# Kernel tuning notes

Hardware: AMD Instinct MI355X
Metric: run time of the kernel (lower is better)

The kernel has to match this reference:

```python
import jax, jax.numpy as jnp
from jax import lax
import numpy as np

N_NODES = 8192
N_FEATURES = 1024
N_FILTRATIONS = 4
HIDDEN_DIM = 64
MAX_DEG = 8            # fixed out-degree used when generating edge_list
N_EDGES = N_NODES * MAX_DEG


def setup_inputs() -> dict:
    key = jax.random.key(0)
    ks = jax.random.split(key, 10)
    X = jax.random.normal(ks[0], (N_NODES, N_FEATURES), dtype=jnp.float32)
    # directed edge list, exactly MAX_DEG out-edges per node
    src = jnp.repeat(jnp.arange(N_NODES, dtype=jnp.int32), MAX_DEG)
    dst = jax.random.randint(ks[1], (N_EDGES,), 0, N_NODES, dtype=jnp.int32)
    edge_list = jnp.stack([src, dst], axis=0)
    # filtrations_nn: Linear(n_features,32) -> ReLU -> Linear(32,n_filtrations)
    W1 = jax.random.normal(ks[2], (32, N_FEATURES), dtype=jnp.float32) * 0.05
    b1 = jnp.zeros((32,), jnp.float32)
    W2 = jax.random.normal(ks[3], (N_FILTRATIONS, 32), dtype=jnp.float32) * 0.05
    b2 = jnp.zeros((N_FILTRATIONS,), jnp.float32)
    # deep sets: theta = Linear(2*n_filtrations, hidden), rho = Linear(1, n_features)
    Wt = jax.random.normal(ks[4], (HIDDEN_DIM, 2 * N_FILTRATIONS), dtype=jnp.float32) * 0.05
    bt = jnp.zeros((HIDDEN_DIM,), jnp.float32)
    Wr = jax.random.normal(ks[5], (N_FEATURES, 1), dtype=jnp.float32) * 0.05
    br = jnp.zeros((N_FEATURES,), jnp.float32)
    return {"X": X, "edge_list": edge_list, "W1": W1, "b1": b1, "W2": W2,
            "b2": b2, "Wt": Wt, "bt": bt, "Wr": Wr, "br": br}


def uf_find(parent, node):
    # chase parent pointers until a root (parent[v] == v)
    return lax.while_loop(lambda v: parent[v] != v, lambda v: parent[v], node)


def build_neighbor_table(edge_list, n_nodes, max_deg):
    # padded CSR-style neighbor table (n_nodes, max_deg), -1 = no edge
    src = edge_list[0].astype(jnp.int32)
    dst = edge_list[1].astype(jnp.int32)
    e = src.shape[0]
    order_e = jnp.argsort(src)  # stable
    src_s, dst_s = src[order_e], dst[order_e]
    counts = jnp.zeros(n_nodes, jnp.int32).at[src].add(1)
    offsets = jnp.concatenate([jnp.zeros(1, jnp.int32), jnp.cumsum(counts)[:-1].astype(jnp.int32)])
    slot = jnp.arange(e, dtype=jnp.int32) - offsets[src_s]
    return jnp.full((n_nodes, max_deg), -1, jnp.int32).at[src_s, slot].set(dst_s)


def persistence_dim0(values, nbr_table):
    """0-dim persistence via sequential union-find with elder rule.
    Row for sort-position j: (birth=j, death=step when the component born at j is absorbed).
    Returned indexed by node id (diagram[order[j]] = row j), matching the torch code."""
    n = values.shape[0]
    order = jnp.argsort(values).astype(jnp.int32)  # filtration order
    pos = jnp.zeros(n, jnp.int32).at[order].set(jnp.arange(n, dtype=jnp.int32))  # rank
    parent0 = jnp.arange(n, dtype=jnp.int32)
    deaths0 = jnp.zeros(n, jnp.float32)

    def step_fn(carry, sv):
        parent, deaths = carry
        s, vertex = sv
        nbrs = nbr_table[vertex]

        def edge_body(k, pc):
            parent, deaths = pc
            u = nbrs[k]
            u_c = jnp.maximum(u, 0)
            valid = (u >= 0) & (pos[u_c] <= s)  # neighbor already activated
            u_eff = jnp.where(valid, u_c, vertex)
            r1 = uf_find(parent, vertex)
            r2 = uf_find(parent, u_eff)
            parent = parent.at[vertex].set(r1).at[u_eff].set(r2)  # path compression
            merge = r1 != r2
            older_is_r1 = pos[r1] < pos[r2]
            absorbed = jnp.where(older_is_r1, r2, r1)   # younger root dies (elder rule)
            survivor = jnp.where(older_is_r1, r1, r2)
            parent = parent.at[absorbed].set(jnp.where(merge, survivor, absorbed))
            dp = pos[absorbed]
            deaths = deaths.at[dp].set(jnp.where(merge, s.astype(jnp.float32), deaths[dp]))
            return (parent, deaths)

        parent, deaths = lax.fori_loop(0, MAX_DEG, edge_body, (parent, deaths))
        return (parent, deaths), None

    (_, deaths), _ = lax.scan(step_fn, (parent0, deaths0),
                              (jnp.arange(n, dtype=jnp.int32), order))
    # finalize: undying components -> inf in the original; use finite cap n for numerics
    deaths = jnp.where(deaths == 0.0, jnp.float32(n), deaths)
    births = jnp.arange(n, dtype=jnp.float32)
    diag_sorted = jnp.stack([births, deaths], axis=1)  # (n, 2), row j = sort position j
    return jnp.zeros((n, 2), jnp.float32).at[order].set(diag_sorted)


def reference(X, edge_list, W1, b1, W2, b2, Wt, bt, Wr, br):
    n = X.shape[0]
    # filtrations_nn
    h = jax.nn.relu(X @ W1.T + b1)
    filt = h @ W2.T + b2                      # (n, n_filtrations)
    filt_ng = lax.stop_gradient(filt)         # diagram is piecewise constant in filt
    nbr_table = build_neighbor_table(edge_list, n, MAX_DEG)
    pds = [persistence_dim0(filt_ng[:, i], nbr_table) for i in range(N_FILTRATIONS)]
    pd = jnp.stack(pds, axis=0).transpose(1, 0, 2).reshape(n, 2 * N_FILTRATIONS)
    # DeepSetsAggregation(theta, rho) with index=zeros(hidden_dim), dim=1:
    theta = pd @ Wt.T + bt                    # (n, hidden)
    pooled = jnp.sum(theta, axis=1, keepdims=True)  # segment-sum of dim 1 into one bucket
    x_hat = pooled @ Wr.T + br                # (n, n_features)
    return X + x_hat
```

## Files before the change

### kernel.cpp

```cpp
#include <hip/hip_runtime.h>

#define N_NODES     8192
#define N_FEAT      1024
#define N_FILT      4
#define MAXDEG      8
#define BLK         256
#define NB          (N_NODES / BLK)

__global__ __launch_bounds__(256) void filt_kernel(
    const float* __restrict__ X, const float* __restrict__ W1,
    const float* __restrict__ b1, const float* __restrict__ W2,
    const float* __restrict__ b2, float* __restrict__ filtT)
{
    const int node = blockIdx.x * 8 + (threadIdx.x >> 5);
    const int h    = threadIdx.x & 31;
    const float* xr = X  + (size_t)node * N_FEAT;
    const float* wr = W1 + (size_t)h    * N_FEAT;
    float acc = 0.f;
    for (int j = 0; j < N_FEAT; j += 4) {
        float4 xv = *reinterpret_cast<const float4*>(xr + j);
        float4 wv = *reinterpret_cast<const float4*>(wr + j);
        acc += xv.x * wv.x + xv.y * wv.y + xv.z * wv.z + xv.w * wv.w;
    }
    float hv = fmaxf(acc + b1[h], 0.f);
    #pragma unroll
    for (int fo = 0; fo < N_FILT; ++fo) {
        float v = hv * W2[fo * 32 + h];
        for (int off = 16; off; off >>= 1) v += __shfl_xor(v, off, 32);
        if (h == 0) filtT[fo * N_NODES + node] = v + b2[fo];
    }
}

__global__ void wsum_kernel(const float* __restrict__ Wt,
                            const float* __restrict__ bt,
                            float* __restrict__ wsum)
{
    int t = threadIdx.x;
    if (t < 8) {
        float s = 0.f;
        for (int hh = 0; hh < 64; ++hh) s += Wt[hh * 8 + t];
        wsum[t] = s;
    } else if (t == 8) {
        float s = 0.f;
        for (int hh = 0; hh < 64; ++hh) s += bt[hh];
        wsum[8] = s;
    }
}

__global__ __launch_bounds__(256) void rank_partial_kernel(
    const float* __restrict__ filtT, unsigned short* __restrict__ partial)
{
    const int b  = blockIdx.x;
    const int f  = b >> 7;
    const int cs = (b >> 5) & 3;
    const int cv = b & 31;
    const int v  = (cv << 8) + threadIdx.x;
    const float myv = filtT[(f << 13) + v];

    __shared__ float4 tile[512];
    const float4* src = reinterpret_cast<const float4*>(filtT + (f << 13) + cs * 2048);
    for (int i = threadIdx.x; i < 512; i += 256) tile[i] = src[i];
    __syncthreads();

    int cnt = 0;
    const int ubase = cs * 2048;
    #pragma unroll 4
    for (int j = 0; j < 512; ++j) {
        float4 wv = tile[j];
        int u = ubase + j * 4;
        cnt += (wv.x < myv) || (wv.x == myv && (u + 0) < v);
        cnt += (wv.y < myv) || (wv.y == myv && (u + 1) < v);
        cnt += (wv.z < myv) || (wv.z == myv && (u + 2) < v);
        cnt += (wv.w < myv) || (wv.w == myv && (u + 3) < v);
    }
    partial[((f * 4 + cs) << 13) + v] = (unsigned short)cnt;
}

__global__ __launch_bounds__(256) void rank_final_kernel(
    const unsigned short* __restrict__ partial,
    unsigned short* __restrict__ pos16, unsigned short* __restrict__ order16)
{
    int g = blockIdx.x * 256 + threadIdx.x;
    int f = g >> 13, v = g & 8191;
    int r = (int)partial[((f * 4 + 0) << 13) + v]
          + (int)partial[((f * 4 + 1) << 13) + v]
          + (int)partial[((f * 4 + 2) << 13) + v]
          + (int)partial[((f * 4 + 3) << 13) + v];
    pos16[(f << 13) + v] = (unsigned short)r;
    order16[(f << 13) + r] = (unsigned short)v;
}

__global__ __launch_bounds__(256) void etable_kernel(
    const unsigned short* __restrict__ order16,
    const unsigned short* __restrict__ pos16,
    const int* __restrict__ edge_dst,
    unsigned short* __restrict__ et)
{
    const int f  = blockIdx.x >> 5;
    const int e0 = ((blockIdx.x & 31) << 11);
    for (int i = threadIdx.x; i < 2048; i += 256) {
        int e = e0 + i;
        int s = e >> 3, k = e & 7;
        int v = (int)order16[(f << 13) + s];
        int u = edge_dst[v * MAXDEG + k];
        int q = (int)pos16[(f << 13) + u];
        et[(size_t)f * (N_NODES * MAXDEG) + e] = (unsigned short)(q < s ? q : s);
    }
}

__device__ __forceinline__ int row8min(int v) {
    int t = min(v, __builtin_amdgcn_mov_dpp(v, 0xB1, 0xF, 0xF, true));
    t = min(t, __builtin_amdgcn_mov_dpp(t, 0x4E, 0xF, 0xF, true));
    t = min(t, __builtin_amdgcn_mov_dpp(t, 0x141, 0xF, 0xF, true));
    return t;
}

__device__ __forceinline__ void chase8m(volatile unsigned int* vpd, int (&pk)[8]) {
    unsigned msk = 0;
    for (;;) {
        bool all = true;
        #pragma unroll
        for (int k = 0; k < 8; ++k) {
            if (!(msk & (1u << k))) {
                int q = (int)(vpd[pk[k]] & 0xffffu);
                if (q == pk[k]) msk |= (1u << k);
                else { pk[k] = q; all = false; }
            }
        }
        if (all) break;
    }
}

__global__ __launch_bounds__(256) void persist_kernel(
    const unsigned short* __restrict__ et,
    const unsigned short* __restrict__ pos16,
    unsigned short* __restrict__ death16)
{
    const int f    = blockIdx.x;
    const int tid  = threadIdx.x;
    const int lane = tid & 63;
    const int w    = tid >> 6;

    __shared__ unsigned int   s_pd[N_NODES];
    __shared__ unsigned short s_r16[2][BLK][8];
    __shared__ unsigned char  s_flag[2][BLK];
    __shared__ unsigned short s_list[2][BLK];
    __shared__ int s_wc[2][4];
    volatile unsigned int* vpd = s_pd;

    for (int v = tid; v < N_NODES; v += 256) s_pd[v] = (unsigned)v;
    __syncthreads();

    const unsigned short* etf = et + (size_t)f * (N_NODES * MAXDEG);

    for (int it = 0; it <= NB; ++it) {
        const int buf = it & 1;

        if (w == 0) {
            if (it > 0) {
                const int pbuf = (it - 1) & 1;
                const int plo  = (it - 1) * BLK;
                const int total = s_wc[pbuf][0] + s_wc[pbuf][1]
                                + s_wc[pbuf][2] + s_wc[pbuf][3];
                const int g    = lane >> 3;
                const int slot = lane & 7;
                for (int base = 0; base < total; base += 8) {
                    int idx = base + g;
                    if (idx >= total) idx = total - 1;
                    const int t = (int)s_list[pbuf][idx];
                    int p = (int)s_r16[pbuf][t][slot];
                    for (;;) {
                        int q = (int)(vpd[p] & 0xffffu);
                        if (__all(q == p)) break;
                        p = q;
                    }
                    const int gmax = (total - base < 8) ? (total - base) : 8;
                    bool kprev = false;
                    for (int gg = 0; gg < gmax; ++gg) {
                        if (kprev) {
                            for (;;) {
                                int q = (int)(vpd[p] & 0xffffu);
                                if (__all(q == p)) break;
                                p = q;
                            }
                        }
                        int m = row8min(p);
                        const bool ing  = (g == gg);
                        const bool kill = ing && (p != m);
                        kprev = (__ballot(kill) != 0ull);
                        if (kill)
                            vpd[p] = (unsigned)m | ((unsigned)(plo + t) << 16);
                    }
                }
            }
        } else if (it < NB) {
            const int lo = it * BLK;
            const int h  = tid - 64;
            #pragma unroll
            for (int rep = 0; rep < 2; ++rep) {
                const int sl = (rep == 0) ? h : (192 + h);
                if (rep == 1 && h >= 64) break;
                const int s = lo + sl;
                uint4 raw = *reinterpret_cast<const uint4*>(etf + (size_t)s * 8);
                int e8[8];
                e8[0] = raw.x & 0xffff; e8[1] = raw.x >> 16;
                e8[2] = raw.y & 0xffff; e8[3] = raw.y >> 16;
                e8[4] = raw.z & 0xffff; e8[5] = raw.z >> 16;
                e8[6] = raw.w & 0xffff; e8[7] = raw.w >> 16;
                int pk[8];
                #pragma unroll
                for (int k = 0; k < 8; ++k) pk[k] = e8[k];
                chase8m(vpd, pk);
                int first = -1; bool same = true;
                #pragma unroll
                for (int k = 0; k < 8; ++k) {
                    if (e8[k] == s) continue;
                    if (first < 0) first = pk[k];
                    else same &= (pk[k] == first);
                }
                if (first < 0) {
                    s_flag[buf][sl] = 0;
                } else if (same) {
                    vpd[s] = (unsigned)first | ((unsigned)s << 16);
                    s_flag[buf][sl] = 0;
                } else {
                    s_flag[buf][sl] = 2;
                    #pragma unroll
                    for (int k = 0; k < 8; ++k)
                        s_r16[buf][sl][k] = (unsigned short)pk[k];
                }
            }
        }
        __syncthreads();

        bool impure = false;
        if (it < NB) {
            const int sl = tid;
            const int s  = it * BLK + sl;
            if (s_flag[buf][sl] == 2) {
                int pk[8];
                #pragma unroll
                for (int k = 0; k < 8; ++k) pk[k] = (int)s_r16[buf][sl][k];
                chase8m(vpd, pk);
                int first = -1; bool same = true; int m = pk[0];
                #pragma unroll
                for (int k = 0; k < 8; ++k) {
                    m = min(m, pk[k]);
                    if (pk[k] == s) continue;
                    if (first < 0) first = pk[k];
                    else same &= (pk[k] == first);
                }
                if (same) {
                    vpd[s] = (unsigned)first | ((unsigned)s << 16);
                } else {
                    impure = true;
                    #pragma unroll
                    for (int k = 0; k < 8; ++k)
                        s_r16[buf][sl][k] = (unsigned short)pk[k];
                    vpd[s] = (unsigned)m | ((unsigned)s << 16);
                }
            }
        }
        unsigned long long bal = __ballot(impure);
        int within = __popcll(bal & ((1ull << lane) - 1ull));
        if (it < NB && lane == 0) s_wc[buf][w] = __popcll(bal);
        __syncthreads();
        if (it < NB && impure) {
            int base = 0;
            #pragma unroll
            for (int i = 0; i < 4; ++i) { if (i < w) base += s_wc[buf][i]; }
            s_list[buf][base + within] = (unsigned short)tid;
        }
        __syncthreads();
    }

    for (int n = tid; n < N_NODES; n += 256) {
        int p = (int)pos16[(f << 13) + n];
        int d = (int)(s_pd[p] >> 16);
        death16[(f << 13) + n] = (unsigned short)(d ? d : N_NODES);
    }
}

__global__ __launch_bounds__(256) void out_kernel(
    const float* __restrict__ X, const float* __restrict__ Wr,
    const float* __restrict__ br,
    const unsigned short* __restrict__ pos16,
    const unsigned short* __restrict__ death16,
    const float* __restrict__ wsum,
    float* __restrict__ out)
{
    const int node = blockIdx.x;
    float pl = wsum[8];
    #pragma unroll
    for (int i = 0; i < N_FILT; ++i) {
        pl += (float)pos16[(i << 13) + node]   * wsum[2 * i + 0]
            + (float)death16[(i << 13) + node] * wsum[2 * i + 1];
    }
    const int fb = threadIdx.x * 4;
    const float4 xv = *reinterpret_cast<const float4*>(X + (size_t)node * N_FEAT + fb);
    const float4 wv = *reinterpret_cast<const float4*>(Wr + fb);
    const float4 bv = *reinterpret_cast<const float4*>(br + fb);
    float4 o;
    o.x = xv.x + pl * wv.x + bv.x;
    o.y = xv.y + pl * wv.y + bv.y;
    o.z = xv.z + pl * wv.z + bv.z;
    o.w = xv.w + pl * wv.w + bv.w;
    *reinterpret_cast<float4*>(out + (size_t)node * N_FEAT + fb) = o;
}

extern "C" void kernel_launch(void* const* d_in, const int* in_sizes, int n_in,
                              void* d_out, int out_size, void* d_ws, size_t ws_size,
                              hipStream_t stream) {
    const float* X  = (const float*)d_in[0];
    const int* edge = (const int*)d_in[1];
    const float* W1 = (const float*)d_in[2];
    const float* b1 = (const float*)d_in[3];
    const float* W2 = (const float*)d_in[4];
    const float* b2 = (const float*)d_in[5];
    const float* Wt = (const float*)d_in[6];
    const float* bt = (const float*)d_in[7];
    const float* Wr = (const float*)d_in[8];
    const float* br = (const float*)d_in[9];

    const int* edge_dst = edge + N_NODES * MAXDEG;

    char* wsb = (char*)d_ws;
    float*          filtT   = (float*)(wsb);
    unsigned short* pos16   = (unsigned short*)(wsb + 131072);
    unsigned short* order16 = (unsigned short*)(wsb + 196608);
    unsigned short* death16 = (unsigned short*)(wsb + 196608);
    unsigned short* partial = (unsigned short*)(wsb + 262144);
    unsigned short* et      = (unsigned short*)(wsb + 262144);
    float*          wsum    = (float*)(wsb + 786432);

    hipLaunchKernelGGL(filt_kernel,  dim3(N_NODES / 8), dim3(256), 0, stream,
                       X, W1, b1, W2, b2, filtT);
    hipLaunchKernelGGL(wsum_kernel,  dim3(1), dim3(64), 0, stream, Wt, bt, wsum);
    hipLaunchKernelGGL(rank_partial_kernel, dim3(512), dim3(256), 0, stream,
                       filtT, partial);
    hipLaunchKernelGGL(rank_final_kernel, dim3(128), dim3(256), 0, stream,
                       partial, pos16, order16);
    hipLaunchKernelGGL(etable_kernel, dim3(4 * 32), dim3(256), 0, stream,
                       order16, pos16, edge_dst, et);
    hipLaunchKernelGGL(persist_kernel, dim3(N_FILT), dim3(256), 0, stream,
                       et, pos16, death16);
    hipLaunchKernelGGL(out_kernel,   dim3(N_NODES), dim3(256), 0, stream,
                       X, Wr, br, pos16, death16, wsum, (float*)d_out);
}
```

Before: 767.5 us.

## Resolve impure merges in parallel with atomicMax claims, serialize only conflicts

Adds a parallel phase to the persistence kernel. Impure vertices (those joining several components) re-chase their roots and then claim the losing roots with atomicMax on a packed value whose high bits hold N_NODES minus the vertex index, so the earliest vertex in the block wins. Vertices from the first conflict onward undo their claims and go to a serial list, which one wavefront then replays one vertex at a time. This replaces the previous grouped kill loop with a mostly parallel path, meant to cut serial union-find work. It adds extra block barriers and atomics per iteration and changes how deaths are encoded.

After: 820.3 us. 1.07x slower.

```diff
diff --git a/kernel.cpp b/kernel.cpp
--- a/kernel.cpp
+++ b/kernel.cpp
@@ -144,8 +144,9 @@
     __shared__ unsigned int   s_pd[N_NODES];
     __shared__ unsigned short s_r16[2][BLK][8];
     __shared__ unsigned char  s_flag[2][BLK];
-    __shared__ unsigned short s_list[2][BLK];
-    __shared__ int s_wc[2][4];
+    __shared__ unsigned short s_fail[2][BLK];
+    __shared__ int s_cnt[2][4];
+    __shared__ int s_mn[4];
     volatile unsigned int* vpd = s_pd;
 
     for (int v = tid; v < N_NODES; v += 256) s_pd[v] = (unsigned)v;
@@ -160,37 +161,20 @@
             if (it > 0) {
                 const int pbuf = (it - 1) & 1;
                 const int plo  = (it - 1) * BLK;
-                const int total = s_wc[pbuf][0] + s_wc[pbuf][1]
-                                + s_wc[pbuf][2] + s_wc[pbuf][3];
-                const int g    = lane >> 3;
-                const int slot = lane & 7;
-                for (int base = 0; base < total; base += 8) {
-                    int idx = base + g;
-                    if (idx >= total) idx = total - 1;
-                    const int t = (int)s_list[pbuf][idx];
-                    int p = (int)s_r16[pbuf][t][slot];
+                const int total = s_cnt[pbuf][0] + s_cnt[pbuf][1]
+                                + s_cnt[pbuf][2] + s_cnt[pbuf][3];
+                for (int i = 0; i < total; ++i) {
+                    const int t  = (int)s_fail[pbuf][i];
+                    const int sv = plo + t;
+                    int p = (int)s_r16[pbuf][t][lane & 7];
                     for (;;) {
                         int q = (int)(vpd[p] & 0xffffu);
                         if (__all(q == p)) break;
                         p = q;
                     }
-                    const int gmax = (total - base < 8) ? (total - base) : 8;
-                    bool kprev = false;
-                    for (int gg = 0; gg < gmax; ++gg) {
-                        if (kprev) {
-                            for (;;) {
-                                int q = (int)(vpd[p] & 0xffffu);
-                                if (__all(q == p)) break;
-                                p = q;
-                            }
-                        }
-                        int m = row8min(p);
-                        const bool ing  = (g == gg);
-                        const bool kill = ing && (p != m);
-                        kprev = (__ballot(kill) != 0ull);
-                        if (kill)
-                            vpd[p] = (unsigned)m | ((unsigned)(plo + t) << 16);
-                    }
+                    int m = row8min(p);
+                    if (lane < 8 && p != m)
+                        vpd[p] = (unsigned)m | ((unsigned)(N_NODES - sv) << 16);
                 }
             }
         } else if (it < NB) {
@@ -221,7 +205,7 @@
                 if (first < 0) {
                     s_flag[buf][sl] = 0;
                 } else if (same) {
-                    vpd[s] = (unsigned)first | ((unsigned)s << 16);
+                    vpd[s] = (unsigned)first | ((unsigned)(N_NODES - s) << 16);
                     s_flag[buf][sl] = 0;
                 } else {
                     s_flag[buf][sl] = 2;
@@ -234,50 +218,107 @@
         __syncthreads();
 
         bool impure = false;
-        if (it < NB) {
-            const int sl = tid;
-            const int s  = it * BLK + sl;
-            if (s_flag[buf][sl] == 2) {
-                int pk[8];
+        int  pk[8];
+        int  m = 0;
+        unsigned enc = 0;
+        const int sl = tid;
+        const int s  = it * BLK + sl;
+        if (it < NB && s_flag[buf][sl] == 2) {
+            #pragma unroll
+            for (int k = 0; k < 8; ++k) pk[k] = (int)s_r16[buf][sl][k];
+            chase8m(vpd, pk);
+            int first = -1; bool same = true; m = pk[0];
+            #pragma unroll
+            for (int k = 0; k < 8; ++k) {
+                m = min(m, pk[k]);
+                if (pk[k] == s) continue;
+                if (first < 0) first = pk[k];
+                else same &= (pk[k] == first);
+            }
+            enc = (unsigned)(N_NODES - s);
+            if (same) {
+                vpd[s] = (unsigned)first | (enc << 16);
+            } else {
+                impure = true;
+                vpd[s] = (unsigned)m | (enc << 16);
+            }
+        }
+        __syncthreads();
+
+        if (impure) {
+            chase8m(vpd, pk);
+            int first = -1; bool same = true; int m2 = pk[0];
+            #pragma unroll
+            for (int k = 0; k < 8; ++k) {
+                m2 = min(m2, pk[k]);
+                if (pk[k] == s) continue;
+                if (first < 0) first = pk[k];
+                else same &= (pk[k] == first);
+            }
+            if (same) {
+                impure = false;
+            } else {
+                m = m2;
                 #pragma unroll
-                for (int k = 0; k < 8; ++k) pk[k] = (int)s_r16[buf][sl][k];
-                chase8m(vpd, pk);
-                int first = -1; bool same = true; int m = pk[0];
-                #pragma unroll
-                for (int k = 0; k < 8; ++k) {
-                    m = min(m, pk[k]);
-                    if (pk[k] == s) continue;
-                    if (first < 0) first = pk[k];
-                    else same &= (pk[k] == first);
-                }
-                if (same) {
-                    vpd[s] = (unsigned)first | ((unsigned)s << 16);
-                } else {
-                    impure = true;
-                    #pragma unroll
-                    for (int k = 0; k < 8; ++k)
-                        s_r16[buf][sl][k] = (unsigned short)pk[k];
-                    vpd[s] = (unsigned)m | ((unsigned)s << 16);
-                }
-            }
-        }
-        unsigned long long bal = __ballot(impure);
-        int within = __popcll(bal & ((1ull << lane) - 1ull));
-        if (it < NB && lane == 0) s_wc[buf][w] = __popcll(bal);
-        __syncthreads();
-        if (it < NB && impure) {
+                for (int k = 0; k < 8; ++k)
+                    s_r16[buf][sl][k] = (unsigned short)pk[k];
+            }
+        }
+        __syncthreads();
+
+        if (impure) {
+            const unsigned val = (unsigned)m | (enc << 16);
+            #pragma unroll
+            for (int k = 0; k < 8; ++k) {
+                int r = pk[k];
+                if (r != s && r != m) atomicMax(&s_pd[r], val);
+            }
+        }
+        __syncthreads();
+
+        bool lost = false;
+        if (impure) {
+            #pragma unroll
+            for (int k = 0; k < 8; ++k) {
+                int r = pk[k];
+                if (r != s && r != m) lost |= ((s_pd[r] >> 16) != enc);
+            }
+        }
+        {
+            unsigned long long bal = __ballot(lost);
+            if (lane == 0)
+                s_mn[w] = bal ? ((int)__builtin_ctzll(bal) + (w << 6)) : 0x7fffffff;
+        }
+        __syncthreads();
+
+        const int sstar = min(min(s_mn[0], s_mn[1]), min(s_mn[2], s_mn[3]));
+        bool failed = impure && (sl >= sstar);
+        if (failed) {
+            #pragma unroll
+            for (int k = 0; k < 8; ++k) {
+                int r = pk[k];
+                if (r != s && r != m && (s_pd[r] >> 16) == enc)
+                    s_pd[r] = (unsigned)r;
+            }
+        }
+        unsigned long long balf = __ballot(failed);
+        int within = __popcll(balf & ((1ull << lane) - 1ull));
+        if (it < NB && lane == 0) s_cnt[buf][w] = __popcll(balf);
+        __syncthreads();
+
+        if (failed) {
             int base = 0;
             #pragma unroll
-            for (int i = 0; i < 4; ++i) { if (i < w) base += s_wc[buf][i]; }
-            s_list[buf][base + within] = (unsigned short)tid;
+            for (int i = 0; i < 4; ++i) { if (i < w) base += s_cnt[buf][i]; }
+            s_fail[buf][base + within] = (unsigned short)sl;
         }
         __syncthreads();
     }
 
     for (int n = tid; n < N_NODES; n += 256) {
         int p = (int)pos16[(f << 13) + n];
-        int d = (int)(s_pd[p] >> 16);
-        death16[(f << 13) + n] = (unsigned short)(d ? d : N_NODES);
+        death16[(f << 13) + n] =
+            (unsigned short)(N_NODES - (int)(s_pd[p] >> 16));
     }
 }
 
```
